# Kernel optimization log

Measured on AMD Instinct MI355X. Metric: run time of the kernel, lower is better.

The kernel has to match this reference:

```python
import jax, jax.numpy as jnp
import numpy as np

DIM = 256
QK = 256
HEADS = 8
NWIN = 16
TOPK = 4
MLP_RATIO = 4
SCALE = QK ** -0.5


def setup_inputs() -> dict:
    key = jax.random.key(0)
    ks = jax.random.split(key, 8)
    p = lambda k, shp: jax.random.normal(k, shp, jnp.float32) * 0.02
    hid = MLP_RATIO * DIM
    return {
        "x": jax.random.normal(ks[0], (8, DIM, 64, 64), jnp.float32),
        # to_q / to_kv : 1x1 Conv2d_BN (eval-mode BN with running stats 0/1 -> scale+shift)
        "wq": p(ks[1], (QK, DIM)), "gq": jnp.ones((QK,), jnp.float32), "bq": jnp.zeros((QK,), jnp.float32),
        "wkv": p(ks[2], (QK + DIM, DIM)), "gkv": jnp.ones((QK + DIM,), jnp.float32), "bkv": jnp.zeros((QK + DIM,), jnp.float32),
        # LEPE depthwise 5x5 conv
        "w_lepe": p(ks[3], (DIM, 1, 5, 5)), "b_lepe": jnp.zeros((DIM,), jnp.float32),
        # Mlp: fc1(1x1 Conv2d_BN) -> dwconv3x3 -> ReLU -> fc2(1x1 Conv2d_BN)
        "w_fc1": p(ks[4], (hid, DIM)), "g_fc1": jnp.ones((hid,), jnp.float32), "b_fc1": jnp.zeros((hid,), jnp.float32),
        "w_dw": p(ks[5], (hid, 1, 3, 3)), "b_dw": jnp.zeros((hid,), jnp.float32),
        "w_fc2": p(ks[6], (DIM, hid)), "g_fc2": jnp.ones((DIM,), jnp.float32), "b_fc2": jnp.zeros((DIM,), jnp.float32),
    }


def _dwconv(x, w, b, pad):
    # x: NCHW, w: (C,1,k,k) depthwise
    out = jax.lax.conv_general_dilated(
        x, w, (1, 1), [(pad, pad), (pad, pad)],
        feature_group_count=x.shape[1],
        dimension_numbers=("NCHW", "OIHW", "NCHW"))
    return out + b[None, :, None, None]


def _bra(x, wq, gq, bq, wkv, gkv, bkv, w_lepe, b_lepe):
    # Bi-Level Routing Attention. x: NCHW
    N, C, H, W = x.shape
    j = i = NWIN
    h, w_ = H // j, W // i          # per-window spatial (4,4)
    p2, w2 = j * i, h * w_          # 256 windows, 16 tokens/window
    xh = x.transpose(0, 2, 3, 1)    # NHWC
    # windowize: (N, p2, h, w, C)
    xw = xh.reshape(N, j, h, i, w_, C).transpose(0, 1, 3, 2, 4, 5).reshape(N, p2, h, w_, C)
    # 1x1 conv + BN(eval: stats 0/1) == matmul * gamma + beta
    q = (xw @ wq.T) * gq + bq                    # (N,p2,h,w,QK)
    kv = (xw @ wkv.T) * gkv + bkv                # (N,p2,h,w,QK+C)
    q_pix = q.reshape(N, p2, w2, QK)
    kv_pix = kv.reshape(N, p2, w2, QK + C)       # identity kv_down
    q_win = q.mean((2, 3))                       # (N,p2,QK)
    k_win = kv[..., :QK].mean((2, 3))            # (N,p2,QK)
    # LEPE on V in full-image layout
    v_img = kv[..., QK:].reshape(N, j, i, h, w_, C).transpose(0, 1, 3, 2, 4, 5).reshape(N, H, W, C)
    lepe = _dwconv(v_img.transpose(0, 3, 1, 2), w_lepe, b_lepe, 2).transpose(0, 2, 3, 1)  # NHWC
    # window-level topk routing (detached, non-differentiable)
    qd = jax.lax.stop_gradient(q_win)
    kd = jax.lax.stop_gradient(k_win)
    logit = (qd * SCALE) @ kd.transpose(0, 2, 1)            # (N,p2,p2)
    _, r_idx = jax.lax.top_k(logit, TOPK)                   # (N,p2,TOPK); r_weight unused (mul_weight='none')
    # gather selected KV windows: (N,p2,TOPK,w2,QK+C)
    kv_sel = jax.vmap(lambda kvp, idx: kvp[idx])(kv_pix, r_idx)
    ch_k, ch_v = QK // HEADS, C // HEADS
    k_sel = kv_sel[..., :QK].reshape(N, p2, TOPK * w2, HEADS, ch_k).transpose(0, 1, 3, 2, 4)
    v_sel = kv_sel[..., QK:].reshape(N, p2, TOPK * w2, HEADS, ch_v).transpose(0, 1, 3, 2, 4)
    qh = q_pix.reshape(N, p2, w2, HEADS, ch_k).transpose(0, 1, 3, 2, 4)
    attn = jax.nn.softmax(jnp.einsum("npmqc,npmkc->npmqk", qh * SCALE, k_sel), axis=-1)
    out = jnp.einsum("npmqk,npmkc->npmqc", attn, v_sel)     # (N,p2,HEADS,w2,ch_v)
    out = out.transpose(0, 1, 3, 2, 4).reshape(N, j, i, h, w_, C)
    out = out.transpose(0, 1, 3, 2, 4, 5).reshape(N, H, W, C)
    out = out + lepe                                         # wo = Identity
    return out.transpose(0, 3, 1, 2)                         # NCHW


def reference(x, wq, gq, bq, wkv, gkv, bkv, w_lepe, b_lepe,
              w_fc1, g_fc1, b_fc1, w_dw, b_dw, w_fc2, g_fc2, b_fc2):
    # top_Block: x = x + attn(x); x = x + mlp(x)   (drop_path inactive in eval)
    x = x + _bra(x, wq, gq, bq, wkv, gkv, bkv, w_lepe, b_lepe)
    h1 = jnp.einsum("nchw,dc->ndhw", x, w_fc1) * g_fc1[None, :, None, None] + b_fc1[None, :, None, None]
    h1 = jax.nn.relu(_dwconv(h1, w_dw, b_dw, 1))
    h2 = jnp.einsum("nchw,dc->ndhw", h1, w_fc2) * g_fc2[None, :, None, None] + b_fc2[None, :, None, None]
    return x + h2
```

## Files before the change

kernel.cpp:

```cpp
#include <hip/hip_runtime.h>
#include <hip/hip_bf16.h>

#define NBATCH 8
#define CDIM 256
#define HH 64
#define WW 64
#define HWSZ 4096
#define TT 32768
#define QKVD 768
#define TOPK 4
#define HID 1024
#define ATTN_SCALE 0.0625f

typedef __hip_bfloat16 bf16;
typedef __attribute__((ext_vector_type(8))) short s8v;
typedef __attribute__((ext_vector_type(4))) float f4v;

__device__ __forceinline__ float toF(bf16 v) { return __bfloat162float(v); }
__device__ __forceinline__ bf16  toB(float v) { return __float2bfloat16(v); }

__device__ __forceinline__ void gload_lds16(const bf16* g, bf16* l) {
    __builtin_amdgcn_global_load_lds(
        (const __attribute__((address_space(1))) void*)g,
        (__attribute__((address_space(3))) void*)l, 16, 0, 0);
}

__global__ void k_prep(const float* __restrict__ wq, const float* __restrict__ gq,
                       const float* __restrict__ wkv, const float* __restrict__ gkv,
                       const float* __restrict__ wfc1, const float* __restrict__ gfc1,
                       const float* __restrict__ wfc2, const float* __restrict__ gfc2,
                       const float* __restrict__ bq, const float* __restrict__ bkv,
                       const float* __restrict__ w_dw, const float* __restrict__ b_dw,
                       bf16* __restrict__ wbqkv, bf16* __restrict__ wbfc1,
                       bf16* __restrict__ wbfc2, float* __restrict__ bias768,
                       float* __restrict__ wdwT) {
    int i = blockIdx.x * 256 + threadIdx.x;
    if (i < 196608) {
        int r = i >> 8;
        float g = (r < 256) ? gq[r] : gkv[r - 256];
        float w = (r < 256) ? wq[i] : wkv[i - 65536];
        wbqkv[i] = toB(w * g);
        if (i < 768) bias768[i] = (i < 256) ? bq[i] : bkv[i - 256];
    } else if (i < 458752) {
        int j = i - 196608;
        wbfc1[j] = toB(wfc1[j] * gfc1[j >> 8]);
    } else if (i < 720896) {
        int j = i - 458752;
        wbfc2[j] = toB(wfc2[j] * gfc2[j >> 10]);
    } else if (i < 731136) {
        int j = i - 720896;
        int cg = j / 80, r = j - cg * 80;
        wdwT[j] = (r < 72) ? w_dw[(cg * 8 + r / 9) * 9 + (r % 9)]
                           : b_dw[cg * 8 + (r - 72)];
    }
}

__global__ void k_xt(const float* __restrict__ x, bf16* __restrict__ xt) {
    __shared__ float tile[32][33];
    int s0 = blockIdx.x * 32, c0 = blockIdx.y * 32, n = blockIdx.z;
    int tx = threadIdx.x, ty = threadIdx.y;
#pragma unroll
    for (int r = 0; r < 4; r++)
        tile[ty + r * 8][tx] = x[(size_t)n * CDIM * HWSZ + (size_t)(c0 + ty + r * 8) * HWSZ + s0 + tx];
    __syncthreads();
#pragma unroll
    for (int r = 0; r < 4; r++)
        xt[((size_t)n * HWSZ + s0 + ty + r * 8) * CDIM + c0 + tx] = toB(tile[tx][ty + r * 8]);
}

__global__ void k_xwin(const float* __restrict__ x, float* __restrict__ xwin) {
    int b = blockIdx.x;
    int n = b >> 8, c = b & 255;
    int p = threadIdx.x, wy = p >> 4, wx = p & 15;
    const float* pl = x + ((size_t)n * CDIM + c) * HWSZ;
    float s = 0.f;
#pragma unroll
    for (int dy = 0; dy < 4; dy++)
#pragma unroll
        for (int dx = 0; dx < 4; dx++)
            s += pl[(wy * 4 + dy) * WW + wx * 4 + dx];
    xwin[((size_t)(n << 8) + p) * 256 + c] = s * 0.0625f;
}

__global__ void k_qkwin(const float* __restrict__ xwin,
                        const float* __restrict__ wq, const float* __restrict__ wkv,
                        const float* __restrict__ gq, const float* __restrict__ bq,
                        const float* __restrict__ gkv, const float* __restrict__ bkv,
                        float* __restrict__ qkwin) {
    __shared__ float As[16][68];
    __shared__ float Bs[16][68];
    int m0 = blockIdx.x * 64, n0 = blockIdx.y * 64;
    int tid = threadIdx.x;
    int tx = tid & 15, ty = tid >> 4;
    float acc[4][4] = {};
    for (int k0 = 0; k0 < 256; k0 += 16) {
#pragma unroll
        for (int r = 0; r < 4; r++) {
            int lin = tid + r * 256;
            int row = lin >> 4, kk = lin & 15;
            As[kk][row] = xwin[(size_t)(m0 + row) * 256 + k0 + kk];
            int n = n0 + row;
            const float* wr = (n < 256) ? (wq + (size_t)n * 256) : (wkv + (size_t)(n - 256) * 256);
            Bs[kk][row] = wr[k0 + kk];
        }
        __syncthreads();
#pragma unroll
        for (int kk = 0; kk < 16; kk++) {
            float a[4], bb[4];
#pragma unroll
            for (int i = 0; i < 4; i++) a[i] = As[kk][tx * 4 + i];
#pragma unroll
            for (int j = 0; j < 4; j++) bb[j] = Bs[kk][ty * 4 + j];
#pragma unroll
            for (int i = 0; i < 4; i++)
#pragma unroll
                for (int j = 0; j < 4; j++) acc[i][j] += a[i] * bb[j];
        }
        __syncthreads();
    }
#pragma unroll
    for (int j = 0; j < 4; j++) {
        int n = n0 + ty * 4 + j;
        float gg = (n < 256) ? gq[n] : gkv[n - 256];
        float bb = (n < 256) ? bq[n] : bkv[n - 256];
#pragma unroll
        for (int i = 0; i < 4; i++)
            qkwin[(size_t)(m0 + tx * 4 + i) * 512 + n] = acc[i][j] * gg + bb;
    }
}

__global__ void k_logits(const float* __restrict__ qkwin, float* __restrict__ logits) {
    __shared__ float As[16][68];
    __shared__ float Bs[16][68];
    int m0 = blockIdx.x * 64, n0 = blockIdx.y * 64, img = blockIdx.z;
    const float* base = qkwin + (size_t)(img << 8) * 512;
    int tid = threadIdx.x;
    int tx = tid & 15, ty = tid >> 4;
    float acc[4][4] = {};
    for (int k0 = 0; k0 < 256; k0 += 16) {
#pragma unroll
        for (int r = 0; r < 4; r++) {
            int lin = tid + r * 256;
            int row = lin >> 4, kk = lin & 15;
            As[kk][row] = base[(size_t)(m0 + row) * 512 + k0 + kk];
            Bs[kk][row] = base[(size_t)(n0 + row) * 512 + 256 + k0 + kk];
        }
        __syncthreads();
#pragma unroll
        for (int kk = 0; kk < 16; kk++) {
            float a[4], bb[4];
#pragma unroll
            for (int i = 0; i < 4; i++) a[i] = As[kk][tx * 4 + i];
#pragma unroll
            for (int j = 0; j < 4; j++) bb[j] = Bs[kk][ty * 4 + j];
#pragma unroll
            for (int i = 0; i < 4; i++)
#pragma unroll
                for (int j = 0; j < 4; j++) acc[i][j] += a[i] * bb[j];
        }
        __syncthreads();
    }
    float* Lr = logits + (size_t)(img << 8) * 256;
#pragma unroll
    for (int j = 0; j < 4; j++)
#pragma unroll
        for (int i = 0; i < 4; i++)
            Lr[(size_t)(m0 + tx * 4 + i) * 256 + n0 + ty * 4 + j] = acc[i][j];
}

__global__ __launch_bounds__(256) void k_topk(const float* __restrict__ logits,
                                              int* __restrict__ topk) {
    int row = blockIdx.x * 4 + (threadIdx.x >> 6);
    int lane = threadIdx.x & 63;
    float4 v4 = *(const float4*)(logits + (size_t)row * 256 + lane * 4);
    float v[4] = {v4.x, v4.y, v4.z, v4.w};
#pragma unroll
    for (int sel = 0; sel < TOPK; sel++) {
        float mv = v[0]; int mi = lane * 4;
#pragma unroll
        for (int j = 1; j < 4; j++)
            if (v[j] > mv) { mv = v[j]; mi = lane * 4 + j; }
#pragma unroll
        for (int off = 1; off < 64; off <<= 1) {
            float ov = __shfl_xor(mv, off);
            int oi = __shfl_xor(mi, off);
            if (ov > mv || (ov == mv && oi < mi)) { mv = ov; mi = oi; }
        }
        if (lane == 0) topk[(size_t)row * TOPK + sel] = mi;
        if ((mi >> 2) == lane) v[mi & 3] = -INFINITY;
    }
}

template <int BM, int BN>
__global__ __launch_bounds__(256) void k_mfma(const bf16* __restrict__ A,
                                              const bf16* __restrict__ Wb,
                                              const float* __restrict__ bias,
                                              bf16* __restrict__ out,
                                              int M, int N, int K) {
    constexpr int WROWS = BM / 2, WCOLS = BN / 2;
    constexpr int WM = WROWS / 16, WN = WCOLS / 16;
    constexpr int CA = (BM * 4) / 256;
    constexpr int CB = (BN * 4) / 256;
    __shared__ bf16 As[BM * 32];
    __shared__ bf16 Bs[BN * 32];
    int gx = gridDim.x;
    int lin = blockIdx.x + blockIdx.y * gx;
    int tot = gx * gridDim.y;
    int cpx = tot >> 3;
    int swz = (lin & 7) * cpx + (lin >> 3);
    int m0 = (swz % gx) * BM, n0 = (swz / gx) * BN;
    int tid = threadIdx.x;
    int w = tid >> 6, lane = tid & 63;
    int wr = w >> 1, wc = w & 1;
    int lm = lane & 15, lq = lane >> 4;
    f4v acc[WM][WN];
#pragma unroll
    for (int i = 0; i < WM; i++)
#pragma unroll
        for (int j = 0; j < WN; j++) acc[i][j] = (f4v){0.f, 0.f, 0.f, 0.f};

    for (int k0 = 0; k0 < K; k0 += 32) {
#pragma unroll
        for (int q = 0; q < CA; q++) {
            int c = tid + q * 256, row = c >> 2, col = c & 3;
            gload_lds16(A + (size_t)(m0 + row) * K + k0 + col * 8,
                        As + (size_t)(w * 64 + q * 256) * 8);
        }
#pragma unroll
        for (int q = 0; q < CB; q++) {
            int c = tid + q * 256, row = c >> 2, col = c & 3;
            gload_lds16(Wb + (size_t)(n0 + row) * K + k0 + col * 8,
                        Bs + (size_t)(w * 64 + q * 256) * 8);
        }
        asm volatile("s_waitcnt vmcnt(0)" ::: "memory");
        __syncthreads();
        s8v af[WM], bfr[WN];
#pragma unroll
        for (int i = 0; i < WM; i++)
            af[i] = *(const s8v*)&As[(wr * WROWS + i * 16 + lm) * 32 + lq * 8];
#pragma unroll
        for (int j = 0; j < WN; j++)
            bfr[j] = *(const s8v*)&Bs[(wc * WCOLS + j * 16 + lm) * 32 + lq * 8];
#pragma unroll
        for (int i = 0; i < WM; i++)
#pragma unroll
            for (int j = 0; j < WN; j++)
                acc[i][j] = __builtin_amdgcn_mfma_f32_16x16x32_bf16(af[i], bfr[j], acc[i][j], 0, 0, 0);
        __syncthreads();
    }
#pragma unroll
    for (int j = 0; j < WN; j++) {
        int n = n0 + wc * WCOLS + j * 16 + lm;
        float bb = bias[n];
#pragma unroll
        for (int i = 0; i < WM; i++) {
            int mb = m0 + wr * WROWS + i * 16 + lq * 4;
#pragma unroll
            for (int r = 0; r < 4; r++)
                out[(size_t)(mb + r) * N + n] = toB(acc[i][j][r] + bb);
        }
    }
}

__global__ __launch_bounds__(256) void k_lepe_t(const bf16* __restrict__ qkv,
                                                const float* __restrict__ w_lepe,
                                                const float* __restrict__ b_lepe,
                                                bf16* __restrict__ lepe) {
    __shared__ float lw[25 * 64 * 4];
    int tid = threadIdx.x;
    int cg = tid & 63;
    int slot = tid >> 6;
    int b = blockIdx.x;
    int n = b & 7;
    int bx = b >> 3;
    int y = bx >> 1;
    int x0 = (bx & 1) * 32 + slot * 8;
#pragma unroll
    for (int j = 0; j < 25; j++) {
        int g = tid + j * 256;
        float val = w_lepe[g];
        int ch = g / 25, k = g - ch * 25;
        lw[(k * 64 + (ch >> 2)) * 4 + (ch & 3)] = val;
    }
    float4 b4 = *(const float4*)(b_lepe + cg * 4);
    const float* bias4 = (const float*)&b4;
    __syncthreads();
    const bf16* vb = qkv + (size_t)n * HWSZ * QKVD + 512;
    bf16* dst = lepe + (size_t)n * HWSZ * CDIM;
    float o[8][4];
#pragma unroll
    for (int xi = 0; xi < 8; xi++)
#pragma unroll
        for (int c = 0; c < 4; c++) o[xi][c] = bias4[c];
#pragma unroll
    for (int dy = -2; dy <= 2; dy++) {
        int yy = y + dy;
        if (yy < 0 || yy >= HH) continue;
        float rf[12][4];
#pragma unroll
        for (int ii = 0; ii < 12; ii++) {
            int xx = x0 - 2 + ii;
            if (xx >= 0 && xx < WW) {
                uint2 v = *(const uint2*)(vb + (size_t)(yy * WW + xx) * QKVD + cg * 4);
                const bf16* pv = (const bf16*)&v;
#pragma unroll
                for (int c = 0; c < 4; c++) rf[ii][c] = toF(pv[c]);
            } else {
#pragma unroll
                for (int c = 0; c < 4; c++) rf[ii][c] = 0.f;
            }
        }
#pragma unroll
        for (int dx = 0; dx < 5; dx++) {
            int k = (dy + 2) * 5 + dx;
            float4 w4v = *(const float4*)&lw[(k * 64 + cg) * 4];
            const float* w4 = (const float*)&w4v;
#pragma unroll
            for (int xi = 0; xi < 8; xi++)
#pragma unroll
                for (int c = 0; c < 4; c++) o[xi][c] += rf[xi + dx][c] * w4[c];
        }
    }
#pragma unroll
    for (int xi = 0; xi < 8; xi++) {
        uint2 pk;
        bf16* pb = (bf16*)&pk;
#pragma unroll
        for (int c = 0; c < 4; c++) pb[c] = toB(o[xi][c]);
        *(uint2*)(dst + (size_t)(y * WW + x0 + xi) * CDIM + cg * 4) = pk;
    }
}

__global__ __launch_bounds__(256) void k_attn(const bf16* __restrict__ qkv,
                                              const int* __restrict__ topk,
                                              bf16* __restrict__ attnout) {
    __shared__ bf16 vst[256][72];
    __shared__ bf16 plds[4][16][72];
    __shared__ float lsm[4][16];
    __shared__ int toks[64];
    int b = blockIdx.x;
    int n = b >> 8, p = b & 255;
    int wy = p >> 4, wx = p & 15;
    int tid = threadIdx.x;
    if (tid < 64) {
        int rp = topk[((size_t)(n << 8) + p) * TOPK + (tid >> 4)] & 255;
        int st = tid & 15;
        toks[tid] = ((rp >> 4) * 4 + (st >> 2)) * WW + (rp & 15) * 4 + (st & 3);
    }
    __syncthreads();
    const bf16* qbase = qkv + (size_t)n * HWSZ * QKVD;
    {
        int kt = tid & 63, jj = tid >> 6;
#pragma unroll
        for (int pass = 0; pass < 8; pass++) {
            int d0 = pass * 32 + jj * 8;
            uint4 v = *(const uint4*)(qbase + (size_t)toks[kt] * QKVD + 512 + d0);
            const bf16* pv = (const bf16*)&v;
#pragma unroll
            for (int e = 0; e < 8; e++) vst[d0 + e][kt] = pv[e];
        }
    }
    __syncthreads();
    int w = tid >> 6, lane = tid & 63;
    int ln = lane & 15, lq = lane >> 4;
    int myS = (wy * 4 + (ln >> 2)) * WW + wx * 4 + (ln & 3);
    const f4v fz = {0.f, 0.f, 0.f, 0.f};
    for (int hh = 0; hh < 2; hh++) {
        int h = w * 2 + hh;
        s8v qf = *(const s8v*)(qbase + (size_t)myS * QKVD + h * 32 + lq * 8);
        f4v st4[4];
#pragma unroll
        for (int t = 0; t < 4; t++) {
            s8v kf = *(const s8v*)(qbase + (size_t)toks[t * 16 + ln] * QKVD + 256 + h * 32 + lq * 8);
            st4[t] = __builtin_amdgcn_mfma_f32_16x16x32_bf16(kf, qf, fz, 0, 0, 0);
        }
        float mx = -INFINITY;
#pragma unroll
        for (int t = 0; t < 4; t++)
#pragma unroll
            for (int r = 0; r < 4; r++) mx = fmaxf(mx, st4[t][r]);
        mx = fmaxf(mx, __shfl_xor(mx, 16));
        mx = fmaxf(mx, __shfl_xor(mx, 32));
        mx *= ATTN_SCALE;
        float sum = 0.f;
#pragma unroll
        for (int t = 0; t < 4; t++)
#pragma unroll
            for (int r = 0; r < 4; r++) {
                float pp = __expf(st4[t][r] * ATTN_SCALE - mx);
                sum += pp;
                plds[w][ln][t * 16 + lq * 4 + r] = toB(pp);
            }
        sum += __shfl_xor(sum, 16);
        sum += __shfl_xor(sum, 32);
        if (lq == 0) lsm[w][ln] = sum;
        __syncthreads();
        s8v ap0 = *(const s8v*)&plds[w][ln][lq * 8];
        s8v ap1 = *(const s8v*)&plds[w][ln][32 + lq * 8];
#pragma unroll
        for (int dt = 0; dt < 2; dt++) {
            int dim = h * 32 + dt * 16 + ln;
            s8v vv0 = *(const s8v*)&vst[dim][lq * 8];
            s8v vv1 = *(const s8v*)&vst[dim][32 + lq * 8];
            f4v o = __builtin_amdgcn_mfma_f32_16x16x32_bf16(ap0, vv0, fz, 0, 0, 0);
            o = __builtin_amdgcn_mfma_f32_16x16x32_bf16(ap1, vv1, o, 0, 0, 0);
#pragma unroll
            for (int r = 0; r < 4; r++) {
                int t = lq * 4 + r;
                float linv = 1.f / lsm[w][t];
                int s = (wy * 4 + (t >> 2)) * WW + wx * 4 + (t & 3);
                attnout[((size_t)n * HWSZ + s) * CDIM + dim] = toB(o[r] * linv);
            }
        }
        __syncthreads();
    }
}

__global__ __launch_bounds__(256) void k_x1(const bf16* __restrict__ xt,
                                            const bf16* __restrict__ lepe,
                                            const bf16* __restrict__ attnout,
                                            bf16* __restrict__ x1) {
    size_t i = ((size_t)blockIdx.x * 256 + threadIdx.x) * 8;
    uint4 a = *(const uint4*)(xt + i);
    uint4 b = *(const uint4*)(attnout + i);
    uint4 c = *(const uint4*)(lepe + i);
    const bf16* pa = (const bf16*)&a;
    const bf16* pb = (const bf16*)&b;
    const bf16* pc = (const bf16*)&c;
    uint4 r;
    bf16* pr = (bf16*)&r;
#pragma unroll
    for (int e = 0; e < 8; e++) pr[e] = toB(toF(pa[e]) + toF(pb[e]) + toF(pc[e]));
    *(uint4*)(x1 + i) = r;
}

__global__ __launch_bounds__(256) void k_dw3_t(const bf16* __restrict__ h1,
                                               const float* __restrict__ wdwT,
                                               bf16* __restrict__ h1p) {
    int tid = threadIdx.x;
    int cg = tid & 127;
    int slot = tid >> 7;
    int seg = blockIdx.x;
    int img = blockIdx.y;
    int y = seg >> 2;
    int x0 = ((seg & 3) << 4) + (slot << 3);
    const float* wp = wdwT + cg * 80;
    float w[72], bias[8];
#pragma unroll
    for (int i = 0; i < 72; i++) w[i] = wp[i];
#pragma unroll
    for (int c = 0; c < 8; c++) bias[c] = wp[72 + c];
    const uint4* src = (const uint4*)h1 + (size_t)img * HWSZ * 128;
    uint4* dst = (uint4*)h1p + (size_t)img * HWSZ * 128;
#pragma unroll
    for (int xi = 0; xi < 8; xi++) {
        int x = x0 + xi;
        float o[8];
#pragma unroll
        for (int c = 0; c < 8; c++) o[c] = bias[c];
#pragma unroll
        for (int dy = -1; dy <= 1; dy++) {
            int yy = y + dy;
            if (yy < 0 || yy >= HH) continue;
#pragma unroll
            for (int dx = -1; dx <= 1; dx++) {
                int xx = x + dx;
                if (xx < 0 || xx >= WW) continue;
                int k = (dy + 1) * 3 + (dx + 1);
                uint4 v = src[(size_t)(yy * WW + xx) * 128 + cg];
                const bf16* pv = (const bf16*)&v;
#pragma unroll
                for (int c = 0; c < 8; c++) o[c] += toF(pv[c]) * w[c * 9 + k];
            }
        }
        uint4 pk;
        bf16* pb = (bf16*)&pk;
#pragma unroll
        for (int c = 0; c < 8; c++) pb[c] = toB(fmaxf(o[c], 0.f));
        dst[(size_t)(y * WW + x) * 128 + cg] = pk;
    }
}

__global__ void k_final(const bf16* __restrict__ x1, const bf16* __restrict__ h2,
                        float* __restrict__ out) {
    __shared__ float tile[32][33];
    int s0 = blockIdx.x * 32, c0 = blockIdx.y * 32, n = blockIdx.z;
    int tx = threadIdx.x, ty = threadIdx.y;
#pragma unroll
    for (int r = 0; r < 4; r++) {
        int s = s0 + ty + r * 8;
        size_t idx = ((size_t)n * HWSZ + s) * CDIM + c0 + tx;
        tile[tx][ty + r * 8] = toF(x1[idx]) + toF(h2[idx]);
    }
    __syncthreads();
#pragma unroll
    for (int r = 0; r < 4; r++) {
        int c = c0 + ty + r * 8;
        out[(size_t)n * CDIM * HWSZ + (size_t)c * HWSZ + s0 + tx] = tile[ty + r * 8][tx];
    }
}

extern "C" void kernel_launch(void* const* d_in, const int* in_sizes, int n_in,
                              void* d_out, int out_size, void* d_ws, size_t ws_size,
                              hipStream_t stream) {
    (void)in_sizes; (void)n_in; (void)out_size; (void)ws_size;
    const float* x      = (const float*)d_in[0];
    const float* wq     = (const float*)d_in[1];
    const float* gq     = (const float*)d_in[2];
    const float* bq     = (const float*)d_in[3];
    const float* wkv    = (const float*)d_in[4];
    const float* gkv    = (const float*)d_in[5];
    const float* bkv    = (const float*)d_in[6];
    const float* w_lepe = (const float*)d_in[7];
    const float* b_lepe = (const float*)d_in[8];
    const float* w_fc1  = (const float*)d_in[9];
    const float* g_fc1  = (const float*)d_in[10];
    const float* b_fc1  = (const float*)d_in[11];
    const float* w_dw   = (const float*)d_in[12];
    const float* b_dw   = (const float*)d_in[13];
    const float* w_fc2  = (const float*)d_in[14];
    const float* g_fc2  = (const float*)d_in[15];
    const float* b_fc2  = (const float*)d_in[16];

    char* ws = (char*)d_ws;
    bf16*  qkv    = (bf16*)(ws);
    bf16*  lepe   = (bf16*)(ws + 50331648);
    bf16*  attn   = (bf16*)(ws + 67108864);
    bf16*  xt     = (bf16*)(ws + 83886080);
    bf16*  x1     = (bf16*)(ws + 83886080);
    bf16*  h1     = (bf16*)(ws);
    bf16*  h1p    = (bf16*)(ws + 33554432);
    bf16*  h2     = (bf16*)(ws + 67108864);
    float* xwin   = (float*)(ws + 100663296);
    float* qkwin  = (float*)(ws + 102760448);
    int*   tk     = (int*)(ws + 106954752);
    bf16*  wbqkv  = (bf16*)(ws + 106987520);
    bf16*  wbfc1  = (bf16*)(ws + 107380736);
    bf16*  wbfc2  = (bf16*)(ws + 107905024);
    float* bias768= (float*)(ws + 108429312);
    float* wdwT   = (float*)(ws + 108433408);
    float* logits = (float*)(ws + 108478464);

    k_prep<<<2856, 256, 0, stream>>>(wq, gq, wkv, gkv, w_fc1, g_fc1, w_fc2, g_fc2,
                                     bq, bkv, w_dw, b_dw,
                                     wbqkv, wbfc1, wbfc2, bias768, wdwT);
    k_xt<<<dim3(128, 8, 8), dim3(32, 8), 0, stream>>>(x, xt);
    k_xwin<<<2048, 256, 0, stream>>>(x, xwin);
    k_qkwin<<<dim3(32, 8), 256, 0, stream>>>(xwin, wq, wkv, gq, bq, gkv, bkv, qkwin);
    k_logits<<<dim3(4, 4, 8), 256, 0, stream>>>(qkwin, logits);
    k_topk<<<512, 256, 0, stream>>>(logits, tk);
    k_mfma<128, 128><<<dim3(256, 6), 256, 0, stream>>>(
        xt, wbqkv, bias768, qkv, TT, QKVD, CDIM);
    k_lepe_t<<<1024, 256, 0, stream>>>(qkv, w_lepe, b_lepe, lepe);
    k_attn<<<2048, 256, 0, stream>>>(qkv, tk, attn);
    k_x1<<<4096, 256, 0, stream>>>(xt, lepe, attn, x1);
    for (int c = 0; c < 2; c++) {
        bf16* x1c = x1 + (size_t)c * 16384 * CDIM;
        bf16* h2c = h2 + (size_t)c * 16384 * CDIM;
        k_mfma<128, 128><<<dim3(128, 8), 256, 0, stream>>>(
            x1c, wbfc1, b_fc1, h1, 16384, HID, CDIM);
        k_dw3_t<<<dim3(256, 4), 256, 0, stream>>>(h1, wdwT, h1p);
        k_mfma<64, 128><<<dim3(256, 2), 256, 0, stream>>>(
            h1p, wbfc2, b_fc2, h2c, 16384, CDIM, HID);
    }
    k_final<<<dim3(128, 8, 8), dim3(32, 8), 0, stream>>>(x1, h2, (float*)d_out);
}
```

Baseline: 429.8 us.

## Fuse residual add into attention and run MLP over full batch in one pass

The residual plus LEPE add is folded into the attention epilogue, which now updates x1 in place and removes the separate k_x1 kernel and its attention-output buffer. The workspace is re-laid out so the MLP's h1/h1p/h2 buffers cover all 8 images, letting the two-chunk MLP loop collapse into single fc1, dwconv and fc2 launches. Block indexing in attention and dwconv is interleaved across images. This cuts launches and one full-tensor round trip through memory, at the cost of a larger workspace and scalar read-modify-write traffic in the attention epilogue.

```diff
diff --git a/kernel.cpp b/kernel.cpp
--- a/kernel.cpp
+++ b/kernel.cpp
@@ -333,13 +333,14 @@
 
 __global__ __launch_bounds__(256) void k_attn(const bf16* __restrict__ qkv,
                                               const int* __restrict__ topk,
-                                              bf16* __restrict__ attnout) {
+                                              const bf16* __restrict__ lepe,
+                                              bf16* x1t) {
     __shared__ bf16 vst[256][72];
     __shared__ bf16 plds[4][16][72];
     __shared__ float lsm[4][16];
     __shared__ int toks[64];
     int b = blockIdx.x;
-    int n = b >> 8, p = b & 255;
+    int n = b & 7, p = b >> 3;
     int wy = p >> 4, wx = p & 15;
     int tid = threadIdx.x;
     if (tid < 64) {
@@ -409,29 +410,12 @@
                 int t = lq * 4 + r;
                 float linv = 1.f / lsm[w][t];
                 int s = (wy * 4 + (t >> 2)) * WW + wx * 4 + (t & 3);
-                attnout[((size_t)n * HWSZ + s) * CDIM + dim] = toB(o[r] * linv);
+                size_t idx = ((size_t)n * HWSZ + s) * CDIM + dim;
+                x1t[idx] = toB(o[r] * linv + toF(x1t[idx]) + toF(lepe[idx]));
             }
         }
         __syncthreads();
     }
-}
-
-__global__ __launch_bounds__(256) void k_x1(const bf16* __restrict__ xt,
-                                            const bf16* __restrict__ lepe,
-                                            const bf16* __restrict__ attnout,
-                                            bf16* __restrict__ x1) {
-    size_t i = ((size_t)blockIdx.x * 256 + threadIdx.x) * 8;
-    uint4 a = *(const uint4*)(xt + i);
-    uint4 b = *(const uint4*)(attnout + i);
-    uint4 c = *(const uint4*)(lepe + i);
-    const bf16* pa = (const bf16*)&a;
-    const bf16* pb = (const bf16*)&b;
-    const bf16* pc = (const bf16*)&c;
-    uint4 r;
-    bf16* pr = (bf16*)&r;
-#pragma unroll
-    for (int e = 0; e < 8; e++) pr[e] = toB(toF(pa[e]) + toF(pb[e]) + toF(pc[e]));
-    *(uint4*)(x1 + i) = r;
 }
 
 __global__ __launch_bounds__(256) void k_dw3_t(const bf16* __restrict__ h1,
@@ -440,8 +424,9 @@
     int tid = threadIdx.x;
     int cg = tid & 127;
     int slot = tid >> 7;
-    int seg = blockIdx.x;
-    int img = blockIdx.y;
+    int lin = blockIdx.x;
+    int img = lin & 7;
+    int seg = lin >> 3;
     int y = seg >> 2;
     int x0 = ((seg & 3) << 4) + (slot << 3);
     const float* wp = wdwT + cg * 80;
@@ -525,21 +510,20 @@
     char* ws = (char*)d_ws;
     bf16*  qkv    = (bf16*)(ws);
     bf16*  lepe   = (bf16*)(ws + 50331648);
-    bf16*  attn   = (bf16*)(ws + 67108864);
-    bf16*  xt     = (bf16*)(ws + 83886080);
-    bf16*  x1     = (bf16*)(ws + 83886080);
-    bf16*  h1     = (bf16*)(ws);
-    bf16*  h1p    = (bf16*)(ws + 33554432);
-    bf16*  h2     = (bf16*)(ws + 67108864);
-    float* xwin   = (float*)(ws + 100663296);
-    float* qkwin  = (float*)(ws + 102760448);
-    int*   tk     = (int*)(ws + 106954752);
-    bf16*  wbqkv  = (bf16*)(ws + 106987520);
-    bf16*  wbfc1  = (bf16*)(ws + 107380736);
-    bf16*  wbfc2  = (bf16*)(ws + 107905024);
-    float* bias768= (float*)(ws + 108429312);
-    float* wdwT   = (float*)(ws + 108433408);
-    float* logits = (float*)(ws + 108478464);
+    bf16*  xt     = (bf16*)(ws + 67108864);
+    bf16*  x1     = (bf16*)(ws + 67108864);
+    bf16*  h1     = (bf16*)(ws + 83886080);
+    bf16*  h1p    = (bf16*)(ws + 150994944);
+    bf16*  h2     = (bf16*)(ws + 218103808);
+    float* xwin   = (float*)(ws + 234881024);
+    float* qkwin  = (float*)(ws + 236978176);
+    float* logits = (float*)(ws + 241172480);
+    int*   tk     = (int*)(ws + 243269632);
+    bf16*  wbqkv  = (bf16*)(ws + 243302400);
+    bf16*  wbfc1  = (bf16*)(ws + 243695616);
+    bf16*  wbfc2  = (bf16*)(ws + 244219904);
+    float* bias768= (float*)(ws + 244744192);
+    float* wdwT   = (float*)(ws + 244747264);
 
     k_prep<<<2856, 256, 0, stream>>>(wq, gq, wkv, gkv, w_fc1, g_fc1, w_fc2, g_fc2,
                                      bq, bkv, w_dw, b_dw,
@@ -552,16 +536,11 @@
     k_mfma<128, 128><<<dim3(256, 6), 256, 0, stream>>>(
         xt, wbqkv, bias768, qkv, TT, QKVD, CDIM);
     k_lepe_t<<<1024, 256, 0, stream>>>(qkv, w_lepe, b_lepe, lepe);
-    k_attn<<<2048, 256, 0, stream>>>(qkv, tk, attn);
-    k_x1<<<4096, 256, 0, stream>>>(xt, lepe, attn, x1);
-    for (int c = 0; c < 2; c++) {
-        bf16* x1c = x1 + (size_t)c * 16384 * CDIM;
-        bf16* h2c = h2 + (size_t)c * 16384 * CDIM;
-        k_mfma<128, 128><<<dim3(128, 8), 256, 0, stream>>>(
-            x1c, wbfc1, b_fc1, h1, 16384, HID, CDIM);
-        k_dw3_t<<<dim3(256, 4), 256, 0, stream>>>(h1, wdwT, h1p);
-        k_mfma<64, 128><<<dim3(256, 2), 256, 0, stream>>>(
-            h1p, wbfc2, b_fc2, h2c, 16384, CDIM, HID);
-    }
+    k_attn<<<2048, 256, 0, stream>>>(qkv, tk, lepe, x1);
+    k_mfma<128, 128><<<dim3(256, 8), 256, 0, stream>>>(
+        x1, wbfc1, b_fc1, h1, TT, HID, CDIM);
+    k_dw3_t<<<2048, 256, 0, stream>>>(h1, wdwT, h1p);
+    k_mfma<64, 128><<<dim3(512, 2), 256, 0, stream>>>(
+        h1p, wbfc2, b_fc2, h2, TT, CDIM, HID);
     k_final<<<dim3(128, 8, 8), dim3(32, 8), 0, stream>>>(x1, h2, (float*)d_out);
 }
```

Result: faster. 405.6 us (-5.6%).
